# Kernel tuning notes

Hardware: AMD Instinct MI355X
Metric: run time of the kernel (lower is better)

## Reference

```python
import jax, jax.numpy as jnp
import numpy as np

PH, PW = 2, 2  # roi_output_h, roi_output_w


def _make_boxes(k, n):
    xy = jax.random.uniform(k, (n, 4), jnp.float32, 0.0, 7.0)
    x1 = jnp.minimum(xy[:, 0], xy[:, 2]); x2 = jnp.maximum(xy[:, 0], xy[:, 2])
    y1 = jnp.minimum(xy[:, 1], xy[:, 3]); y2 = jnp.maximum(xy[:, 1], xy[:, 3])
    return jnp.stack([x1, y1, x2, y2], axis=1)


def setup_inputs() -> dict:
    key = jax.random.key(0)
    ks = jax.random.split(key, 12)
    B, C, H, W = 8, 1280, 7, 7
    M, N = 2048, 128
    hid, ncls = 256, 20
    feature_map = jax.random.normal(ks[0], (B, C, H, W), jnp.float32)
    proposals = _make_boxes(ks[1], M)
    proposal_batch_ids = jnp.sort(jax.random.randint(ks[2], (M,), 0, B, jnp.int32))
    gt4 = _make_boxes(ks[3], N)
    labels = jax.random.randint(ks[4], (N,), 0, ncls).astype(jnp.float32)
    bboxes = jnp.concatenate([gt4, labels[:, None]], axis=1)
    bbox_batch_ids = jnp.sort(jax.random.randint(ks[5], (N,), 0, B, jnp.int32))
    W1 = 0.02 * jax.random.normal(ks[6], (C, hid), jnp.float32)
    b1 = jnp.zeros((hid,), jnp.float32)
    W2 = 0.02 * jax.random.normal(ks[7], (hid, hid), jnp.float32)
    b2 = jnp.zeros((hid,), jnp.float32)
    Wcls = 0.02 * jax.random.normal(ks[8], (hid, ncls + 1), jnp.float32)
    bcls = jnp.zeros((ncls + 1,), jnp.float32)
    Wdet = 0.02 * jax.random.normal(ks[9], (hid, 4), jnp.float32)
    bdet = jnp.zeros((4,), jnp.float32)
    return {"feature_map": feature_map, "proposals": proposals, "bboxes": bboxes,
            "W1": W1, "b1": b1, "W2": W2, "b2": b2, "Wcls": Wcls, "bcls": bcls,
            "Wdet": Wdet, "bdet": bdet,
            "proposal_batch_ids": proposal_batch_ids, "bbox_batch_ids": bbox_batch_ids}


def roi_pool(feat, rois, batch_ids, ph, pw):
    """torchvision.ops.roi_pool with spatial_scale=1.0 (quantized max pool)."""
    B, C, H, W = feat.shape
    M = rois.shape[0]
    r = jnp.round(rois)
    x1, y1, x2, y2 = r[:, 0], r[:, 1], r[:, 2], r[:, 3]
    roi_w = jnp.maximum(x2 - x1 + 1.0, 1.0)
    roi_h = jnp.maximum(y2 - y1 + 1.0, 1.0)
    bin_w = roi_w / pw
    bin_h = roi_h / ph
    rf = feat[batch_ids]                      # (M, C, H, W) irregular gather
    ys = jnp.arange(H, dtype=jnp.float32)
    xs = jnp.arange(W, dtype=jnp.float32)
    neg = jnp.float32(-jnp.inf)
    outs = []
    for i in range(ph):
        hs = jnp.clip(jnp.floor(i * bin_h) + y1, 0.0, H)
        he = jnp.clip(jnp.ceil((i + 1) * bin_h) + y1, 0.0, H)
        for j in range(pw):
            ws = jnp.clip(jnp.floor(j * bin_w) + x1, 0.0, W)
            we = jnp.clip(jnp.ceil((j + 1) * bin_w) + x1, 0.0, W)
            ymask = (ys[None, :] >= hs[:, None]) & (ys[None, :] < he[:, None])  # (M,H)
            xmask = (xs[None, :] >= ws[:, None]) & (xs[None, :] < we[:, None])  # (M,W)
            mask = ymask[:, None, :, None] & xmask[:, None, None, :]            # (M,1,H,W)
            m = jnp.where(mask, rf, neg).max(axis=(2, 3))                       # (M,C)
            empty = (he <= hs) | (we <= ws)
            outs.append(jnp.where(empty[:, None], 0.0, m))
    return jnp.stack(outs, axis=-1).reshape(M, C, ph, pw)


def pairwise_iou(p, g):
    """p: (M,4), g: (N,4) -> (M,N) IoU."""
    ix = jnp.clip(jnp.minimum(p[:, None, 2], g[None, :, 2]) - jnp.maximum(p[:, None, 0], g[None, :, 0]), 0.0)
    iy = jnp.clip(jnp.minimum(p[:, None, 3], g[None, :, 3]) - jnp.maximum(p[:, None, 1], g[None, :, 1]), 0.0)
    inter = ix * iy
    ap = (p[:, 2] - p[:, 0]) * (p[:, 3] - p[:, 1])
    ag = (g[:, 2] - g[:, 0]) * (g[:, 3] - g[:, 1])
    union = jnp.maximum(ap[:, None] + ag[None, :] - inter, 1e-6)
    return inter / union


def reference(feature_map, proposals, bboxes, W1, b1, W2, b2, Wcls, bcls, Wdet, bdet,
              proposal_batch_ids, bbox_batch_ids):
    # ROI pool + spatial mean
    roi_feat = roi_pool(feature_map, proposals, proposal_batch_ids, PH, PW)  # (M,C,2,2)
    roi_feat = roi_feat.mean(axis=(2, 3))                                    # (M,C)
    # small MLP head (dropout = identity in deterministic/eval reference)
    h = jax.nn.relu(roi_feat @ W1 + b1)
    h = h @ W2 + b2
    bbox_result = h @ Wdet + bdet   # (M,4)
    cls_result = h @ Wcls + bcls    # (M,21)
    # per-image IoU label assignment, vectorized: mask cross-image pairs
    iou = pairwise_iou(proposals, bboxes[:, :4])                              # (M,N)
    same_img = proposal_batch_ids[:, None] == bbox_batch_ids[None, :]
    iou = jnp.where(same_img, iou, 0.0)
    max_iou = iou.max(axis=1)                                                 # (M,)
    return cls_result, bbox_result, max_iou
```

## Files before the change

### kernel.cpp

```cpp
#include <hip/hip_runtime.h>
#include <math.h>

constexpr int B_ = 8, C_ = 1280, H_ = 7, W_ = 7;
constexpr int M_ = 2048, N_ = 128, HID = 256, NC = 21;
constexpr int DET_OFF = M_ * NC;
constexpr int IOU_OFF = M_ * NC + M_ * 4;
constexpr int NRECT = 784;

typedef __attribute__((ext_vector_type(8))) short bf16x8;
typedef __attribute__((ext_vector_type(8))) unsigned short u16x8;
typedef __attribute__((ext_vector_type(4))) float f32x4;

constexpr size_t W1T_OFF = 0;
constexpr size_t W2T_OFF = W1T_OFF + 655360;
constexpr size_t WHT_OFF = W2T_OFF + 131072;
constexpr size_t AM_OFF  = WHT_OFF + 16384;

constexpr int RECT_BLKS    = B_ * 40;
constexpr int PREP_W1_BLKS = 160;
constexpr int PREP_W2_BLKS = 32;
constexpr int PREP_WH_BLKS = 4;
constexpr int AUX_BLKS = RECT_BLKS + PREP_W1_BLKS + PREP_W2_BLKS + PREP_WH_BLKS;

__device__ __forceinline__ unsigned short f2bf(float f) {
    unsigned u = __builtin_bit_cast(unsigned, f);
    u += 0x7FFFu + ((u >> 16) & 1u);
    return (unsigned short)(u >> 16);
}
__device__ __forceinline__ float bf2f(unsigned short u) {
    return __builtin_bit_cast(float, (unsigned)u << 16);
}
__device__ __forceinline__ int ivix(int s, int e) {
    return s * 7 - ((s * (s - 1)) >> 1) + (e - s - 1);
}

__global__ __launch_bounds__(256) void k_aux(
    const float* __restrict__ fmap,
    const float* __restrict__ W1, const float* __restrict__ W2,
    const float* __restrict__ Wc, const float* __restrict__ Wd,
    unsigned short* __restrict__ allmax, unsigned short* __restrict__ W1t,
    unsigned short* __restrict__ W2t,    unsigned short* __restrict__ Wht)
{
    __shared__ __align__(16) float tile[32 * 49];
    __shared__ __align__(16) unsigned short rect_lds[NRECT][36];

    const int tid = threadIdx.x;
    const int b = blockIdx.x;

    if (b < RECT_BLKS) {
        int img = b / 40, c0 = (b % 40) * 32;
        const float* src = fmap + ((size_t)img * C_ + c0) * 49;
        for (int i4 = tid; i4 < 392; i4 += 256)
            *(float4*)&tile[i4 * 4] = *(const float4*)(src + i4 * 4);
        __syncthreads();

        int c = tid >> 3, sy = tid & 7;
        if (sy < 7) {
            const float* tc = tile + c * 49;
            float colacc[7];
            #pragma unroll
            for (int x = 0; x < 7; ++x) colacc[x] = -INFINITY;
            for (int ey = sy + 1; ey <= 7; ++ey) {
                int y = ey - 1;
                #pragma unroll
                for (int x = 0; x < 7; ++x)
                    colacc[x] = fmaxf(colacc[x], tc[y * 7 + x]);
                int yi = ivix(sy, ey);
                int xi = 0;
                #pragma unroll
                for (int sx = 0; sx < 7; ++sx) {
                    float mx = -INFINITY;
                    #pragma unroll
                    for (int ex = sx + 1; ex <= 7; ++ex) {
                        mx = fmaxf(mx, colacc[ex - 1]);
                        rect_lds[yi * 28 + xi][c] = f2bf(mx);
                        ++xi;
                    }
                }
            }
        }
        __syncthreads();

        unsigned short* dst = allmax + (size_t)img * NRECT * C_ + c0;
        for (int i = tid; i < NRECT * 4; i += 256) {
            int rid = i >> 2, ch = (i & 3) * 8;
            ushort4 lo = *(const ushort4*)&rect_lds[rid][ch];
            ushort4 hi = *(const ushort4*)&rect_lds[rid][ch + 4];
            unsigned short* dp = dst + (size_t)rid * C_ + ch;
            *(ushort4*)dp = lo;
            *(ushort4*)(dp + 4) = hi;
        }
    } else if (b < RECT_BLKS + PREP_W1_BLKS) {
        int k0 = (b - RECT_BLKS) * 8;
        int col = tid;
        u16x8 o;
        #pragma unroll
        for (int j = 0; j < 8; ++j) o[j] = f2bf(W1[(size_t)(k0 + j) * HID + col]);
        *(u16x8*)(W1t + (size_t)col * C_ + k0) = o;
    } else if (b < RECT_BLKS + PREP_W1_BLKS + PREP_W2_BLKS) {
        int k0 = (b - RECT_BLKS - PREP_W1_BLKS) * 8;
        int col = tid;
        u16x8 o;
        #pragma unroll
        for (int j = 0; j < 8; ++j) o[j] = f2bf(W2[(size_t)(k0 + j) * HID + col]);
        *(u16x8*)(W2t + (size_t)col * HID + k0) = o;
    } else {
        int i = (b - RECT_BLKS - PREP_W1_BLKS - PREP_W2_BLKS) * 256 + tid;
        int o32 = i & 31;
        int k0  = (i >> 5) * 8;
        u16x8 o;
        #pragma unroll
        for (int j = 0; j < 8; ++j) {
            float v = 0.0f;
            if (o32 < NC) v = Wc[(size_t)(k0 + j) * NC + o32];
            else if (o32 < NC + 4) v = Wd[(size_t)(k0 + j) * 4 + (o32 - NC)];
            o[j] = f2bf(v);
        }
        *(u16x8*)(Wht + (size_t)o32 * HID + k0) = o;
    }
}

__global__ __launch_bounds__(512) void k_fc(
    const unsigned short* __restrict__ allmax,
    const unsigned short* __restrict__ W1t,
    const unsigned short* __restrict__ W2t,
    const unsigned short* __restrict__ Wht,
    const float* __restrict__ b1v, const float* __restrict__ b2v,
    const float* __restrict__ bc,  const float* __restrict__ bd,
    const float* __restrict__ props, const int* __restrict__ pbid,
    const float* __restrict__ bbx,   const int* __restrict__ gbid,
    float* __restrict__ out)
{
    __shared__ unsigned short featL[8][1288];
    __shared__ unsigned short h1s[16][264];
    __shared__ unsigned short h2s[16][264];
    __shared__ float gbox[N_][4];
    __shared__ int   gids[N_];

    const int tid = threadIdx.x;
    const int row0 = blockIdx.x * 8;

    if (tid < N_) {
        gbox[tid][0] = bbx[tid * 5 + 0];
        gbox[tid][1] = bbx[tid * 5 + 1];
        gbox[tid][2] = bbx[tid * 5 + 2];
        gbox[tid][3] = bbx[tid * 5 + 3];
        gids[tid] = gbid[tid];
    }

    {
        int p = tid >> 6, lane = tid & 63;
        int m = row0 + p;
        float4 bx = *(const float4*)(props + (size_t)m * 4);
        float x1 = rintf(bx.x), y1 = rintf(bx.y);
        float x2 = rintf(bx.z), y2 = rintf(bx.w);
        float rw = fmaxf(x2 - x1 + 1.0f, 1.0f);
        float rh = fmaxf(y2 - y1 + 1.0f, 1.0f);
        float bw = rw * 0.5f, bh = rh * 0.5f;
        int hs0 = __builtin_amdgcn_readfirstlane((int)fminf(fmaxf(y1, 0.f), 7.f));
        int he0 = __builtin_amdgcn_readfirstlane((int)fminf(fmaxf(ceilf(bh) + y1, 0.f), 7.f));
        int hs1 = __builtin_amdgcn_readfirstlane((int)fminf(fmaxf(floorf(bh) + y1, 0.f), 7.f));
        int he1 = __builtin_amdgcn_readfirstlane((int)fminf(fmaxf(ceilf(2.f * bh) + y1, 0.f), 7.f));
        int ws0 = __builtin_amdgcn_readfirstlane((int)fminf(fmaxf(x1, 0.f), 7.f));
        int we0 = __builtin_amdgcn_readfirstlane((int)fminf(fmaxf(ceilf(bw) + x1, 0.f), 7.f));
        int ws1 = __builtin_amdgcn_readfirstlane((int)fminf(fmaxf(floorf(bw) + x1, 0.f), 7.f));
        int we1 = __builtin_amdgcn_readfirstlane((int)fminf(fmaxf(ceilf(2.f * bw) + x1, 0.f), 7.f));
        int bid = __builtin_amdgcn_readfirstlane(pbid[m]);

        int v00 = (he0 > hs0) & (we0 > ws0);
        int v01 = (he0 > hs0) & (we1 > ws1);
        int v10 = (he1 > hs1) & (we0 > ws0);
        int v11 = (he1 > hs1) & (we1 > ws1);
        int yi0 = v00 | v01 ? ivix(hs0, max(he0, hs0 + 1)) : 0;
        int yi1 = v10 | v11 ? ivix(hs1, max(he1, hs1 + 1)) : 0;
        int xi0 = v00 | v10 ? ivix(ws0, max(we0, ws0 + 1)) : 0;
        int xi1 = v01 | v11 ? ivix(ws1, max(we1, ws1 + 1)) : 0;
        const unsigned short* base = allmax + (size_t)bid * NRECT * C_;
        const unsigned short* a00 = base + (size_t)(yi0 * 28 + xi0) * C_;
        const unsigned short* a01 = base + (size_t)(yi0 * 28 + xi1) * C_;
        const unsigned short* a10 = base + (size_t)(yi1 * 28 + xi0) * C_;
        const unsigned short* a11 = base + (size_t)(yi1 * 28 + xi1) * C_;
        float m00 = v00 ? 0.25f : 0.0f;
        float m01 = v01 ? 0.25f : 0.0f;
        float m10 = v10 ? 0.25f : 0.0f;
        float m11 = v11 ? 0.25f : 0.0f;

        for (int it = 0; it < 5; ++it) {
            int c = it * 256 + lane * 4;
            ushort4 u0 = *(const ushort4*)(a00 + c);
            ushort4 u1 = *(const ushort4*)(a01 + c);
            ushort4 u2 = *(const ushort4*)(a10 + c);
            ushort4 u3 = *(const ushort4*)(a11 + c);
            ushort4 o;
            o.x = f2bf(bf2f(u0.x) * m00 + bf2f(u1.x) * m01 + bf2f(u2.x) * m10 + bf2f(u3.x) * m11);
            o.y = f2bf(bf2f(u0.y) * m00 + bf2f(u1.y) * m01 + bf2f(u2.y) * m10 + bf2f(u3.y) * m11);
            o.z = f2bf(bf2f(u0.z) * m00 + bf2f(u1.z) * m01 + bf2f(u2.z) * m10 + bf2f(u3.z) * m11);
            o.w = f2bf(bf2f(u0.w) * m00 + bf2f(u1.w) * m01 + bf2f(u2.w) * m10 + bf2f(u3.w) * m11);
            *(ushort4*)&featL[p][c] = o;
        }
    }
    __syncthreads();

    const int w = tid >> 6, lane = tid & 63;
    const int r = lane & 15, g = lane >> 4;
    const int col0 = w * 32;

    f32x4 acc0 = (f32x4){0.f, 0.f, 0.f, 0.f};
    f32x4 acc1 = (f32x4){0.f, 0.f, 0.f, 0.f};
    const unsigned short* arp = featL[r & 7] + g * 8;
    const unsigned short* bp0 = W1t + (size_t)(col0 + r) * C_ + g * 8;
    const unsigned short* bp1 = bp0 + 16 * C_;

    bf16x8 aA = *(const bf16x8*)arp;
    bf16x8 bA0 = *(const bf16x8*)bp0;
    bf16x8 bA1 = *(const bf16x8*)bp1;
    bf16x8 aB = *(const bf16x8*)(arp + 32);
    bf16x8 bB0 = *(const bf16x8*)(bp0 + 32);
    bf16x8 bB1 = *(const bf16x8*)(bp1 + 32);
    for (int ks = 2; ks < 40; ++ks) {
        bf16x8 aN  = *(const bf16x8*)(arp + ks * 32);
        bf16x8 bN0 = *(const bf16x8*)(bp0 + ks * 32);
        bf16x8 bN1 = *(const bf16x8*)(bp1 + ks * 32);
        acc0 = __builtin_amdgcn_mfma_f32_16x16x32_bf16(aA, bA0, acc0, 0, 0, 0);
        acc1 = __builtin_amdgcn_mfma_f32_16x16x32_bf16(aA, bA1, acc1, 0, 0, 0);
        aA = aB; bA0 = bB0; bA1 = bB1;
        aB = aN; bB0 = bN0; bB1 = bN1;
    }
    acc0 = __builtin_amdgcn_mfma_f32_16x16x32_bf16(aA, bA0, acc0, 0, 0, 0);
    acc1 = __builtin_amdgcn_mfma_f32_16x16x32_bf16(aA, bA1, acc1, 0, 0, 0);
    acc0 = __builtin_amdgcn_mfma_f32_16x16x32_bf16(aB, bB0, acc0, 0, 0, 0);
    acc1 = __builtin_amdgcn_mfma_f32_16x16x32_bf16(aB, bB1, acc1, 0, 0, 0);

    {
        int colA = col0 + r, colB = col0 + 16 + r;
        float biasA = b1v[colA], biasB = b1v[colB];
        #pragma unroll
        for (int i = 0; i < 4; ++i) {
            h1s[g * 4 + i][colA] = f2bf(fmaxf(acc0[i] + biasA, 0.f));
            h1s[g * 4 + i][colB] = f2bf(fmaxf(acc1[i] + biasB, 0.f));
        }
    }
    __syncthreads();

    f32x4 c0v = (f32x4){0.f, 0.f, 0.f, 0.f};
    f32x4 c1v = (f32x4){0.f, 0.f, 0.f, 0.f};
    const unsigned short* bq0 = W2t + (size_t)(col0 + r) * HID + g * 8;
    const unsigned short* bq1 = bq0 + 16 * HID;
    #pragma unroll
    for (int ks = 0; ks < 8; ++ks) {
        bf16x8 a  = *(const bf16x8*)(&h1s[r][ks * 32 + g * 8]);
        bf16x8 u0 = *(const bf16x8*)(bq0 + ks * 32);
        bf16x8 u1 = *(const bf16x8*)(bq1 + ks * 32);
        c0v = __builtin_amdgcn_mfma_f32_16x16x32_bf16(a, u0, c0v, 0, 0, 0);
        c1v = __builtin_amdgcn_mfma_f32_16x16x32_bf16(a, u1, c1v, 0, 0, 0);
    }
    {
        int colA = col0 + r, colB = col0 + 16 + r;
        float biasA = b2v[colA], biasB = b2v[colB];
        #pragma unroll
        for (int i = 0; i < 4; ++i) {
            h2s[g * 4 + i][colA] = f2bf(c0v[i] + biasA);
            h2s[g * 4 + i][colB] = f2bf(c1v[i] + biasB);
        }
    }
    __syncthreads();

    if (w == 0) {
        f32x4 acc3[2];
        #pragma unroll
        for (int f = 0; f < 2; ++f) acc3[f] = (f32x4){0.f, 0.f, 0.f, 0.f};
        const unsigned short* bp3 = Wht + (size_t)r * HID + g * 8;
        #pragma unroll
        for (int ks = 0; ks < 8; ++ks) {
            bf16x8 a = *(const bf16x8*)(&h2s[r][ks * 32 + g * 8]);
            #pragma unroll
            for (int f = 0; f < 2; ++f) {
                bf16x8 b = *(const bf16x8*)(bp3 + (size_t)f * 16 * HID + ks * 32);
                acc3[f] = __builtin_amdgcn_mfma_f32_16x16x32_bf16(a, b, acc3[f], 0, 0, 0);
            }
        }
        if (g < 2) {
            #pragma unroll
            for (int f = 0; f < 2; ++f) {
                int col = f * 16 + r;
                #pragma unroll
                for (int i = 0; i < 4; ++i) {
                    int m = row0 + g * 4 + i;
                    if (col < NC)
                        out[(size_t)m * NC + col] = acc3[f][i] + bc[col];
                    else if (col < NC + 4)
                        out[DET_OFF + (size_t)m * 4 + (col - NC)] = acc3[f][i] + bd[col - NC];
                }
            }
        }
    }

    {
        int m = row0 + w;
        float4 bxp = *(const float4*)(props + (size_t)m * 4);
        float ap2 = (bxp.z - bxp.x) * (bxp.w - bxp.y);
        int pb = pbid[m];
        float best = 0.0f;
        for (int n = lane; n < N_; n += 64) {
            if (gids[n] == pb) {
                float ix = fmaxf(fminf(bxp.z, gbox[n][2]) - fmaxf(bxp.x, gbox[n][0]), 0.0f);
                float iy = fmaxf(fminf(bxp.w, gbox[n][3]) - fmaxf(bxp.y, gbox[n][1]), 0.0f);
                float inter = ix * iy;
                float ag = (gbox[n][2] - gbox[n][0]) * (gbox[n][3] - gbox[n][1]);
                float un = fmaxf(ap2 + ag - inter, 1e-6f);
                best = fmaxf(best, inter / un);
            }
        }
        #pragma unroll
        for (int off = 32; off; off >>= 1)
            best = fmaxf(best, __shfl_xor(best, off));
        if (lane == 0) out[IOU_OFF + m] = best;
    }
}

extern "C" void kernel_launch(void* const* d_in, const int* in_sizes, int n_in,
                              void* d_out, int out_size, void* d_ws, size_t ws_size,
                              hipStream_t stream) {
    const float* fmap  = (const float*)d_in[0];
    const float* props = (const float*)d_in[1];
    const float* bbx   = (const float*)d_in[2];
    const float* W1    = (const float*)d_in[3];
    const float* b1v   = (const float*)d_in[4];
    const float* W2    = (const float*)d_in[5];
    const float* b2v   = (const float*)d_in[6];
    const float* Wc    = (const float*)d_in[7];
    const float* bc    = (const float*)d_in[8];
    const float* Wd    = (const float*)d_in[9];
    const float* bd    = (const float*)d_in[10];
    const int*   pbid  = (const int*)d_in[11];
    const int*   gbid  = (const int*)d_in[12];
    float* out = (float*)d_out;

    char* ws = (char*)d_ws;
    unsigned short* W1t    = (unsigned short*)(ws + W1T_OFF);
    unsigned short* W2t    = (unsigned short*)(ws + W2T_OFF);
    unsigned short* Wht    = (unsigned short*)(ws + WHT_OFF);
    unsigned short* allmax = (unsigned short*)(ws + AM_OFF);

    k_aux<<<dim3(AUX_BLKS), dim3(256), 0, stream>>>(
        fmap, W1, W2, Wc, Wd, allmax, W1t, W2t, Wht);
    k_fc<<<dim3(M_ / 8), dim3(512), 0, stream>>>(
        allmax, W1t, W2t, Wht, b1v, b2v, bc, bd, props, pbid, bbx, gbid, out);
}
```

Measured before the change: 44.49 us.

## Split FC output columns across 16 waves and deepen W1 load pipeline

```diff
diff --git a/kernel.cpp b/kernel.cpp
--- a/kernel.cpp
+++ b/kernel.cpp
@@ -120,7 +120,7 @@
     }
 }
 
-__global__ __launch_bounds__(512) void k_fc(
+__global__ __launch_bounds__(1024) void k_fc(
     const unsigned short* __restrict__ allmax,
     const unsigned short* __restrict__ W1t,
     const unsigned short* __restrict__ W2t,
@@ -148,7 +148,7 @@
         gids[tid] = gbid[tid];
     }
 
-    {
+    if (tid < 512) {
         int p = tid >> 6, lane = tid & 63;
         int m = row0 + p;
         float4 bx = *(const float4*)(props + (size_t)m * 4);
@@ -185,6 +185,7 @@
         float m10 = v10 ? 0.25f : 0.0f;
         float m11 = v11 ? 0.25f : 0.0f;
 
+        #pragma unroll
         for (int it = 0; it < 5; ++it) {
             int c = it * 256 + lane * 4;
             ushort4 u0 = *(const ushort4*)(a00 + c);
@@ -203,65 +204,56 @@
 
     const int w = tid >> 6, lane = tid & 63;
     const int r = lane & 15, g = lane >> 4;
-    const int col0 = w * 32;
-
-    f32x4 acc0 = (f32x4){0.f, 0.f, 0.f, 0.f};
-    f32x4 acc1 = (f32x4){0.f, 0.f, 0.f, 0.f};
+    const int col0 = w * 16;
+
+    f32x4 acc = (f32x4){0.f, 0.f, 0.f, 0.f};
     const unsigned short* arp = featL[r & 7] + g * 8;
-    const unsigned short* bp0 = W1t + (size_t)(col0 + r) * C_ + g * 8;
-    const unsigned short* bp1 = bp0 + 16 * C_;
-
-    bf16x8 aA = *(const bf16x8*)arp;
-    bf16x8 bA0 = *(const bf16x8*)bp0;
-    bf16x8 bA1 = *(const bf16x8*)bp1;
-    bf16x8 aB = *(const bf16x8*)(arp + 32);
-    bf16x8 bB0 = *(const bf16x8*)(bp0 + 32);
-    bf16x8 bB1 = *(const bf16x8*)(bp1 + 32);
-    for (int ks = 2; ks < 40; ++ks) {
-        bf16x8 aN  = *(const bf16x8*)(arp + ks * 32);
-        bf16x8 bN0 = *(const bf16x8*)(bp0 + ks * 32);
-        bf16x8 bN1 = *(const bf16x8*)(bp1 + ks * 32);
-        acc0 = __builtin_amdgcn_mfma_f32_16x16x32_bf16(aA, bA0, acc0, 0, 0, 0);
-        acc1 = __builtin_amdgcn_mfma_f32_16x16x32_bf16(aA, bA1, acc1, 0, 0, 0);
-        aA = aB; bA0 = bB0; bA1 = bB1;
-        aB = aN; bB0 = bN0; bB1 = bN1;
-    }
-    acc0 = __builtin_amdgcn_mfma_f32_16x16x32_bf16(aA, bA0, acc0, 0, 0, 0);
-    acc1 = __builtin_amdgcn_mfma_f32_16x16x32_bf16(aA, bA1, acc1, 0, 0, 0);
-    acc0 = __builtin_amdgcn_mfma_f32_16x16x32_bf16(aB, bB0, acc0, 0, 0, 0);
-    acc1 = __builtin_amdgcn_mfma_f32_16x16x32_bf16(aB, bB1, acc1, 0, 0, 0);
+    const unsigned short* bp  = W1t + (size_t)(col0 + r) * C_ + g * 8;
+
+    bf16x8 af[4], bf[4];
+    #pragma unroll
+    for (int i = 0; i < 4; ++i) {
+        af[i] = *(const bf16x8*)(arp + i * 32);
+        bf[i] = *(const bf16x8*)(bp  + i * 32);
+    }
+    #pragma unroll
+    for (int ks = 4; ks < 40; ++ks) {
+        int sl = ks & 3;
+        acc = __builtin_amdgcn_mfma_f32_16x16x32_bf16(af[sl], bf[sl], acc, 0, 0, 0);
+        af[sl] = *(const bf16x8*)(arp + ks * 32);
+        bf[sl] = *(const bf16x8*)(bp  + ks * 32);
+    }
+    #pragma unroll
+    for (int ks = 40; ks < 44; ++ks)
+        acc = __builtin_amdgcn_mfma_f32_16x16x32_bf16(af[ks & 3], bf[ks & 3], acc, 0, 0, 0);
 
     {
-        int colA = col0 + r, colB = col0 + 16 + r;
-        float biasA = b1v[colA], biasB = b1v[colB];
-        #pragma unroll
-        for (int i = 0; i < 4; ++i) {
-            h1s[g * 4 + i][colA] = f2bf(fmaxf(acc0[i] + biasA, 0.f));
-            h1s[g * 4 + i][colB] = f2bf(fmaxf(acc1[i] + biasB, 0.f));
-        }
-    }
+        int col = col0 + r;
+        float bias = b1v[col];
+        #pragma unroll
+        for (int i = 0; i < 4; ++i)
+            h1s[g * 4 + i][col] = f2bf(fmaxf(acc[i] + bias, 0.f));
+    }
+
+    const unsigned short* bq = W2t + (size_t)(col0 + r) * HID + g * 8;
+    bf16x8 u[8];
+    #pragma unroll
+    for (int ks = 0; ks < 8; ++ks) u[ks] = *(const bf16x8*)(bq + ks * 32);
+
     __syncthreads();
 
-    f32x4 c0v = (f32x4){0.f, 0.f, 0.f, 0.f};
-    f32x4 c1v = (f32x4){0.f, 0.f, 0.f, 0.f};
-    const unsigned short* bq0 = W2t + (size_t)(col0 + r) * HID + g * 8;
-    const unsigned short* bq1 = bq0 + 16 * HID;
+    f32x4 c2 = (f32x4){0.f, 0.f, 0.f, 0.f};
     #pragma unroll
     for (int ks = 0; ks < 8; ++ks) {
-        bf16x8 a  = *(const bf16x8*)(&h1s[r][ks * 32 + g * 8]);
-        bf16x8 u0 = *(const bf16x8*)(bq0 + ks * 32);
-        bf16x8 u1 = *(const bf16x8*)(bq1 + ks * 32);
-        c0v = __builtin_amdgcn_mfma_f32_16x16x32_bf16(a, u0, c0v, 0, 0, 0);
-        c1v = __builtin_amdgcn_mfma_f32_16x16x32_bf16(a, u1, c1v, 0, 0, 0);
+        bf16x8 a = *(const bf16x8*)(&h1s[r][ks * 32 + g * 8]);
+        c2 = __builtin_amdgcn_mfma_f32_16x16x32_bf16(a, u[ks], c2, 0, 0, 0);
     }
     {
-        int colA = col0 + r, colB = col0 + 16 + r;
-        float biasA = b2v[colA], biasB = b2v[colB];
-        #pragma unroll
-        for (int i = 0; i < 4; ++i) {
-            h2s[g * 4 + i][colA] = f2bf(c0v[i] + biasA);
-            h2s[g * 4 + i][colB] = f2bf(c1v[i] + biasB);
-        }
+        int col = col0 + r;
+        float bias = b2v[col];
+        #pragma unroll
+        for (int i = 0; i < 4; ++i)
+            h2s[g * 4 + i][col] = f2bf(c2[i] + bias);
     }
     __syncthreads();
 
@@ -295,7 +287,7 @@
         }
     }
 
-    {
+    if (w < 8) {
         int m = row0 + w;
         float4 bxp = *(const float4*)(props + (size_t)m * 4);
         float ap2 = (bxp.z - bxp.x) * (bxp.w - bxp.y);
@@ -344,6 +336,6 @@
 
     k_aux<<<dim3(AUX_BLKS), dim3(256), 0, stream>>>(
         fmap, W1, W2, Wc, Wd, allmax, W1t, W2t, Wht);
-    k_fc<<<dim3(M_ / 8), dim3(512), 0, stream>>>(
+    k_fc<<<dim3(M_ / 8), dim3(1024), 0, stream>>>(
         allmax, W1t, W2t, Wht, b1v, b2v, bc, bd, props, pbid, bbx, gbid, out);
 }
```

New measurement: 44.23 us, median of 2. Within noise of the previous version (-0.6%).
